# Optimization experiments

Hardware: AMD Instinct MI355X
Metric: run time of the kernel (lower is better)

Reference implementation:

```python
import jax, jax.numpy as jnp
import numpy as np

N_NODES = 100000
N_EDGES = 3200000
IN_CH = 128
HID = 8
HEADS = 8
NEG_SLOPE = 0.2  # PyG GATConv default


def setup_inputs() -> dict:
    key = jax.random.key(0)
    ks = jax.random.split(key, 12)
    s = 0.1
    return {
        "x": jax.random.normal(ks[0], (N_NODES, IN_CH), jnp.float32),
        "edge_index": jax.random.randint(ks[1], (2, N_EDGES), 0, N_NODES, dtype=jnp.int64),
        "W1": jax.random.normal(ks[2], (IN_CH, HEADS * HID), jnp.float32) * s,
        "a_src1": jax.random.normal(ks[3], (1, HEADS, HID), jnp.float32) * s,
        "a_dst1": jax.random.normal(ks[4], (1, HEADS, HID), jnp.float32) * s,
        "b1": jax.random.normal(ks[5], (HEADS * HID,), jnp.float32) * s,
        "W2": jax.random.normal(ks[6], (HEADS * HID, HID), jnp.float32) * s,
        "a_src2": jax.random.normal(ks[7], (1, 1, HID), jnp.float32) * s,
        "a_dst2": jax.random.normal(ks[8], (1, 1, HID), jnp.float32) * s,
        "b2": jax.random.normal(ks[9], (HID,), jnp.float32) * s,
        "Wc": jax.random.normal(ks[10], (HID, 2), jnp.float32) * s,
        "bc": jax.random.normal(ks[11], (2,), jnp.float32) * s,
    }


def gat_conv(x, src, dst, W, a_src, a_dst, b, concat):
    """PyG-style GATConv (eval mode, self-loops already appended to src/dst)."""
    n = x.shape[0]
    H, C = a_src.shape[1], a_src.shape[2]
    h = (x @ W).reshape(n, H, C)                       # [N,H,C]
    alpha_src = jnp.sum(h * a_src, axis=-1)            # [N,H]
    alpha_dst = jnp.sum(h * a_dst, axis=-1)            # [N,H]
    e = jax.nn.leaky_relu(alpha_src[src] + alpha_dst[dst], NEG_SLOPE)  # [E,H]
    # segment softmax over destination-node neighborhoods
    m = jax.ops.segment_max(e, dst, num_segments=n)    # [N,H]
    m = jnp.where(jnp.isfinite(m), m, 0.0)
    p = jnp.exp(e - m[dst])
    z = jax.ops.segment_sum(p, dst, num_segments=n)    # [N,H]
    alpha = p / (z[dst] + 1e-16)                       # [E,H]
    out = jax.ops.segment_sum(alpha[..., None] * h[src], dst, num_segments=n)  # [N,H,C]
    out = out.reshape(n, H * C) if concat else out.mean(axis=1)
    return out + b


def reference(x, edge_index, W1, a_src1, a_dst1, b1, W2, a_src2, a_dst2, b2, Wc, bc):
    n = x.shape[0]
    loops = jnp.arange(n, dtype=edge_index.dtype)
    src = jnp.concatenate([edge_index[0], loops])
    dst = jnp.concatenate([edge_index[1], loops])
    h = jax.nn.relu(gat_conv(x, src, dst, W1, a_src1, a_dst1, b1, concat=True))
    embeddings = gat_conv(h, src, dst, W2, a_src2, a_dst2, b2, concat=False)
    logits = embeddings @ Wc + bc
    return embeddings, logits
```

## Files before the change

### kernel.cpp

```cpp
#include <hip/hip_runtime.h>
#include <hip/hip_bf16.h>

#define NN 100000
#define IN_CH 128
#define HID 8
#define HEADS 8
#define HC 64
#define BSH 8
#define NBUCK ((NN + 255) >> 8)
#define NBLK 512
#define LOG2E 1.44269504088896340736f

__device__ __forceinline__ unsigned short f2bf(float f) {
    unsigned u = __float_as_uint(f);
    unsigned r = (u + 0x7fffu + ((u >> 16) & 1u)) >> 16;
    return (unsigned short)r;
}


__global__ __launch_bounds__(256) void k_bincount(const int* __restrict__ ei, int E, int ET,
                                                  int cpb, int* __restrict__ cnt) {
    __shared__ int h[NBUCK];
    for (int i = threadIdx.x; i < NBUCK; i += 256) h[i] = 0;
    __syncthreads();
    int beg = blockIdx.x * cpb, end = min(ET, beg + cpb);
    for (int t = beg + threadIdx.x; t < end; t += 256) {
        int d = (t < E) ? ei[E + t] : (t - E);
        atomicAdd(&h[d >> BSH], 1);
    }
    __syncthreads();
    for (int i = threadIdx.x; i < NBUCK; i += 256) cnt[i * NBLK + blockIdx.x] = h[i];
}

__global__ __launch_bounds__(256) void k_colscan(int* __restrict__ cnt, int* __restrict__ btot) {
    __shared__ int sd[256];
    int t = threadIdx.x;
    int* col = cnt + blockIdx.x * NBLK;
    int v0 = col[2 * t], v1 = col[2 * t + 1];
    int s = v0 + v1;
    sd[t] = s;
    __syncthreads();
    for (int off = 1; off < 256; off <<= 1) {
        int u = (t >= off) ? sd[t - off] : 0;
        __syncthreads();
        sd[t] += u;
        __syncthreads();
    }
    int excl = sd[t] - s;
    col[2 * t] = excl;
    col[2 * t + 1] = excl + v0;
    if (t == 255) btot[blockIdx.x] = excl + s;
}

__global__ __launch_bounds__(256) void k_bucketbase(const int* __restrict__ btot,
                                                    int* __restrict__ bbase,
                                                    int* __restrict__ row_ptr) {
    __shared__ int sd[256];
    int t = threadIdx.x;
    int v0 = (2 * t < NBUCK) ? btot[2 * t] : 0;
    int v1 = (2 * t + 1 < NBUCK) ? btot[2 * t + 1] : 0;
    int s = v0 + v1;
    sd[t] = s;
    __syncthreads();
    for (int off = 1; off < 256; off <<= 1) {
        int u = (t >= off) ? sd[t - off] : 0;
        __syncthreads();
        sd[t] += u;
        __syncthreads();
    }
    int excl = sd[t] - s;
    if (2 * t < NBUCK) bbase[2 * t] = excl;
    if (2 * t + 1 < NBUCK) bbase[2 * t + 1] = excl + v0;
    if (t == 255) { bbase[NBUCK] = excl + s; row_ptr[NN] = excl + s; }
}

__global__ __launch_bounds__(256) void k_binscatter(const int* __restrict__ ei, int E, int ET,
                                                    int cpb, const int* __restrict__ cnt,
                                                    const int* __restrict__ bbase,
                                                    int2* __restrict__ pairs) {
    __shared__ int cur[NBUCK];
    for (int i = threadIdx.x; i < NBUCK; i += 256)
        cur[i] = bbase[i] + cnt[i * NBLK + blockIdx.x];
    __syncthreads();
    int beg = blockIdx.x * cpb, end = min(ET, beg + cpb);
    for (int t = beg + threadIdx.x; t < end; t += 256) {
        int s, d;
        if (t < E) { s = ei[t]; d = ei[E + t]; } else { s = t - E; d = t - E; }
        int pos = atomicAdd(&cur[d >> BSH], 1);
        pairs[pos] = make_int2(s, d);
    }
}

__global__ __launch_bounds__(256) void k_bucketscatter(const int2* __restrict__ pairs,
                                                       const int* __restrict__ bbase,
                                                       int* __restrict__ row_ptr,
                                                       int* __restrict__ csr) {
    __shared__ int h[256];
    __shared__ int sd[256];
    int b = blockIdx.x;
    int t = threadIdx.x;
    int beg = bbase[b], end = bbase[b + 1];
    h[t] = 0;
    __syncthreads();
    for (int j = beg + t; j < end; j += 256) {
        int2 p = pairs[j];
        atomicAdd(&h[p.y & 255], 1);
    }
    __syncthreads();
    int v = h[t];
    sd[t] = v;
    __syncthreads();
    for (int off = 1; off < 256; off <<= 1) {
        int u = (t >= off) ? sd[t - off] : 0;
        __syncthreads();
        sd[t] += u;
        __syncthreads();
    }
    int excl = sd[t] - v;
    int node = (b << 8) + t;
    if (node < NN) row_ptr[node] = beg + excl;
    __syncthreads();
    h[t] = beg + excl;
    __syncthreads();
    for (int j = beg + t; j < end; j += 256) {
        int2 p = pairs[j];
        int pos = atomicAdd(&h[p.y & 255], 1);
        csr[pos] = p.x;
    }
}


__global__ __launch_bounds__(256) void k_gemm1(const float* __restrict__ x,
                                               const float* __restrict__ W1,
                                               const float* __restrict__ aS,
                                               const float* __restrict__ aD,
                                               unsigned short* __restrict__ h1bf,
                                               float* __restrict__ asrc1,
                                               float* __restrict__ adst1) {
    __shared__ float wl[IN_CH * HC];
    int tid = threadIdx.x;
    {
        const float4* Wg4 = (const float4*)W1;
        float4* wl4 = (float4*)wl;
#pragma unroll
        for (int i = 0; i < 8; ++i) wl4[tid + i * 256] = Wg4[tid + i * 256];
    }
    __syncthreads();
    int lane = tid & 63;
    int row = blockIdx.x * 16 + (tid >> 6) * 4 + (lane >> 4);
    int c0 = (lane & 15) * 4;
    const float4* xr = (const float4*)(x + (size_t)row * IN_CH);
    float4 acc = make_float4(0.f, 0.f, 0.f, 0.f);
#pragma unroll 4
    for (int kq = 0; kq < IN_CH / 4; ++kq) {
        float4 xv = xr[kq];
        const float4* wrow = (const float4*)(wl + (kq * 4) * HC + c0);
        float4 w0 = wrow[0];
        float4 w1 = wrow[HC / 4];
        float4 w2 = wrow[2 * (HC / 4)];
        float4 w3 = wrow[3 * (HC / 4)];
        acc.x += xv.x * w0.x + xv.y * w1.x + xv.z * w2.x + xv.w * w3.x;
        acc.y += xv.x * w0.y + xv.y * w1.y + xv.z * w2.y + xv.w * w3.y;
        acc.z += xv.x * w0.z + xv.y * w1.z + xv.z * w2.z + xv.w * w3.z;
        acc.w += xv.x * w0.w + xv.y * w1.w + xv.z * w2.w + xv.w * w3.w;
    }
    ushort4 hb;
    hb.x = f2bf(acc.x); hb.y = f2bf(acc.y); hb.z = f2bf(acc.z); hb.w = f2bf(acc.w);
    *(ushort4*)(h1bf + (size_t)row * HC + c0) = hb;
    int head = (lane & 15) >> 1;
    int cl = c0 & 7;
    const float* as = aS + head * 8 + cl;
    const float* ad = aD + head * 8 + cl;
    float ps = acc.x * as[0] + acc.y * as[1] + acc.z * as[2] + acc.w * as[3];
    float pd = acc.x * ad[0] + acc.y * ad[1] + acc.z * ad[2] + acc.w * ad[3];
    ps += __shfl_xor(ps, 1, 64);
    pd += __shfl_xor(pd, 1, 64);
    if ((lane & 1) == 0) {
        asrc1[row * 8 + head] = ps * LOG2E;
        adst1[row * 8 + head] = pd * LOG2E;
    }
}


__global__ __launch_bounds__(256) void k_agg1(const int* __restrict__ row_ptr,
                                              const int* __restrict__ csr,
                                              const float* __restrict__ asrc1,
                                              const float* __restrict__ adst1,
                                              const unsigned short* __restrict__ h1bf,
                                              const float* __restrict__ b1,
                                              const float* __restrict__ W2,
                                              const float* __restrict__ aS2,
                                              const float* __restrict__ aD2,
                                              float* __restrict__ h2,
                                              float* __restrict__ asrc2,
                                              float* __restrict__ adst2) {
    int tid = threadIdx.x;
    int lane = tid & 63;
    int slot = lane >> 3;
    int hl = lane & 7;
    float w2r[8];
#pragma unroll
    for (int i = 0; i < 8; ++i) w2r[i] = W2[(hl * 8 + i) * 8 + slot];
    float4 b0 = *(const float4*)(b1 + hl * 8);
    float4 b1v = *(const float4*)(b1 + hl * 8 + 4);
    float as2 = aS2[slot], ad2 = aD2[slot];
    const float4* h1v = (const float4*)h1bf;
    int nbase = (blockIdx.x * 4 + (tid >> 6)) * 4;
    for (int ni = 0; ni < 4; ++ni) {
        int n = nbase + ni;
        float adst = adst1[n * 8 + hl];
        int beg = row_ptr[n], end = row_ptr[n + 1];
        int nit = (end - beg + 7) >> 3;
        float z = 0.f;
        float4 accA = make_float4(0.f, 0.f, 0.f, 0.f);
        float4 accB = make_float4(0.f, 0.f, 0.f, 0.f);
        int j0 = beg + slot;
        bool v0 = j0 < end;
        int s0 = v0 ? csr[j0] : 0;
        int j1 = j0 + 8;
        bool v1 = j1 < end;
        int s1 = v1 ? csr[j1] : 0;
        float a0 = asrc1[(size_t)s0 * 8 + hl];
        float4 r0 = h1v[(size_t)s0 * 8 + hl];
        int jn = j1;
        for (int it = 0; it < nit; ++it) {
            int j2 = jn + 8;
            bool v2 = j2 < end;
            int s2 = v2 ? csr[j2] : 0;
            float a1 = asrc1[(size_t)s1 * 8 + hl];
            float4 r1 = h1v[(size_t)s1 * 8 + hl];
            float e = a0 + adst;
            e = fmaxf(e, 0.2f * e);
            float p = v0 ? exp2f(e) : 0.f;
            unsigned ux = __float_as_uint(r0.x), uy = __float_as_uint(r0.y);
            unsigned uz = __float_as_uint(r0.z), uw = __float_as_uint(r0.w);
            z += p;
            accA.x += p * __uint_as_float(ux << 16);
            accA.y += p * __uint_as_float(ux & 0xffff0000u);
            accA.z += p * __uint_as_float(uy << 16);
            accA.w += p * __uint_as_float(uy & 0xffff0000u);
            accB.x += p * __uint_as_float(uz << 16);
            accB.y += p * __uint_as_float(uz & 0xffff0000u);
            accB.z += p * __uint_as_float(uw << 16);
            accB.w += p * __uint_as_float(uw & 0xffff0000u);
            v0 = v1; a0 = a1; r0 = r1;
            v1 = v2; s1 = s2;
            jn = j2;
        }
#pragma unroll
        for (int off = 8; off <= 32; off <<= 1) {
            z += __shfl_xor(z, off, 64);
            accA.x += __shfl_xor(accA.x, off, 64);
            accA.y += __shfl_xor(accA.y, off, 64);
            accA.z += __shfl_xor(accA.z, off, 64);
            accA.w += __shfl_xor(accA.w, off, 64);
            accB.x += __shfl_xor(accB.x, off, 64);
            accB.y += __shfl_xor(accB.y, off, 64);
            accB.z += __shfl_xor(accB.z, off, 64);
            accB.w += __shfl_xor(accB.w, off, 64);
        }
        float inv = 1.f / (z + 1e-16f);
        float hr0 = fmaxf(accA.x * inv + b0.x, 0.f);
        float hr1 = fmaxf(accA.y * inv + b0.y, 0.f);
        float hr2 = fmaxf(accA.z * inv + b0.z, 0.f);
        float hr3 = fmaxf(accA.w * inv + b0.w, 0.f);
        float hr4 = fmaxf(accB.x * inv + b1v.x, 0.f);
        float hr5 = fmaxf(accB.y * inv + b1v.y, 0.f);
        float hr6 = fmaxf(accB.z * inv + b1v.z, 0.f);
        float hr7 = fmaxf(accB.w * inv + b1v.w, 0.f);
        float part = hr0 * w2r[0] + hr1 * w2r[1] + hr2 * w2r[2] + hr3 * w2r[3] +
                     hr4 * w2r[4] + hr5 * w2r[5] + hr6 * w2r[6] + hr7 * w2r[7];
        part += __shfl_xor(part, 1, 64);
        part += __shfl_xor(part, 2, 64);
        part += __shfl_xor(part, 4, 64);
        if (hl == 0) {
            h2[(size_t)n * 8 + slot] = part;
            float s2v = part * as2;
            float d2v = part * ad2;
            s2v += __shfl_xor(s2v, 8, 64);
            s2v += __shfl_xor(s2v, 16, 64);
            s2v += __shfl_xor(s2v, 32, 64);
            d2v += __shfl_xor(d2v, 8, 64);
            d2v += __shfl_xor(d2v, 16, 64);
            d2v += __shfl_xor(d2v, 32, 64);
            if (slot == 0) {
                asrc2[n] = s2v * LOG2E;
                adst2[n] = d2v * LOG2E;
            }
        }
    }
}


__global__ __launch_bounds__(256) void k_agg2(const int* __restrict__ row_ptr,
                                              const int* __restrict__ csr,
                                              const float* __restrict__ asrc2,
                                              const float* __restrict__ adst2,
                                              const float* __restrict__ h2,
                                              const float* __restrict__ b2,
                                              const float* __restrict__ Wc,
                                              const float* __restrict__ bc,
                                              float* __restrict__ out) {
    int tid = threadIdx.x;
    int lane = tid & 63;
    int n = blockIdx.x * 4 + (tid >> 6);
    int slot = lane >> 3;
    int sl = lane & 7;
    float adst = adst2[n];
    int beg = row_ptr[n], end = row_ptr[n + 1];
    int nit = (end - beg + 7) >> 3;
    float z = 0.f, acc = 0.f;
    int j0 = beg + slot;
    bool v0 = j0 < end;
    int s0 = v0 ? csr[j0] : 0;
    int j1 = j0 + 8;
    bool v1 = j1 < end;
    int s1 = v1 ? csr[j1] : 0;
    float a0 = asrc2[s0];
    float h0 = h2[(size_t)s0 * HID + sl];
    int jn = j1;
    for (int it = 0; it < nit; ++it) {
        int j2 = jn + 8;
        bool v2 = j2 < end;
        int s2 = v2 ? csr[j2] : 0;
        float a1 = asrc2[s1];
        float h1l = h2[(size_t)s1 * HID + sl];
        float e = a0 + adst;
        e = fmaxf(e, 0.2f * e);
        float p = v0 ? exp2f(e) : 0.f;
        z += p;
        acc += p * h0;
        v0 = v1; a0 = a1; h0 = h1l;
        v1 = v2; s1 = s2;
        jn = j2;
    }
#pragma unroll
    for (int off = 8; off <= 32; off <<= 1) {
        z += __shfl_xor(z, off, 64);
        acc += __shfl_xor(acc, off, 64);
    }
    float emb = acc / (z + 1e-16f) + b2[sl];
    if (slot == 0) out[(size_t)n * HID + sl] = emb;
    float t0 = emb * Wc[sl * 2 + 0];
    float t1 = emb * Wc[sl * 2 + 1];
    t0 += __shfl_xor(t0, 1, 64); t0 += __shfl_xor(t0, 2, 64); t0 += __shfl_xor(t0, 4, 64);
    t1 += __shfl_xor(t1, 1, 64); t1 += __shfl_xor(t1, 2, 64); t1 += __shfl_xor(t1, 4, 64);
    if (lane == 0) {
        out[(size_t)NN * HID + n * 2 + 0] = t0 + bc[0];
        out[(size_t)NN * HID + n * 2 + 1] = t1 + bc[1];
    }
}


extern "C" void kernel_launch(void* const* d_in, const int* in_sizes, int n_in,
                              void* d_out, int out_size, void* d_ws, size_t ws_size,
                              hipStream_t stream) {
    const float* x  = (const float*)d_in[0];
    const int*   ei = (const int*)d_in[1];
    const float* W1 = (const float*)d_in[2];
    const float* aS = (const float*)d_in[3];
    const float* aD = (const float*)d_in[4];
    const float* b1 = (const float*)d_in[5];
    const float* W2 = (const float*)d_in[6];
    const float* aS2 = (const float*)d_in[7];
    const float* aD2 = (const float*)d_in[8];
    const float* b2 = (const float*)d_in[9];
    const float* Wc = (const float*)d_in[10];
    const float* bc = (const float*)d_in[11];

    int E = in_sizes[1] / 2;
    int N = NN;
    int ET = E + N;
    int cpb = (ET + NBLK - 1) / NBLK;

    char* p = (char*)d_ws;
    auto alloc = [&](size_t bytes) -> char* {
        char* r = p;
        p += (bytes + 255) & ~(size_t)255;
        return r;
    };
    unsigned short* h1bf = (unsigned short*)alloc((size_t)N * HC * 2);
    float* asrc1  = (float*)alloc((size_t)N * 8 * 4);
    float* adst1  = (float*)alloc((size_t)N * 8 * 4);
    float* h2     = (float*)alloc((size_t)N * HID * 4);
    float* asrc2  = (float*)alloc((size_t)N * 4);
    float* adst2  = (float*)alloc((size_t)N * 4);
    int*   row_ptr= (int*)alloc((size_t)(N + 1) * 4);
    int*   cnt    = (int*)alloc((size_t)NBUCK * NBLK * 4);
    int*   btot   = (int*)alloc((size_t)NBUCK * 4);
    int*   bbase  = (int*)alloc((size_t)(NBUCK + 1) * 4);
    int*   csr    = (int*)alloc((size_t)ET * 4);
    int2*  pairs  = (int2*)alloc((size_t)ET * 8);

    k_bincount<<<NBLK, 256, 0, stream>>>(ei, E, ET, cpb, cnt);
    k_colscan<<<NBUCK, 256, 0, stream>>>(cnt, btot);
    k_bucketbase<<<1, 256, 0, stream>>>(btot, bbase, row_ptr);
    k_binscatter<<<NBLK, 256, 0, stream>>>(ei, E, ET, cpb, cnt, bbase, pairs);
    k_bucketscatter<<<NBUCK, 256, 0, stream>>>(pairs, bbase, row_ptr, csr);

    k_gemm1<<<N / 16, 256, 0, stream>>>(x, W1, aS, aD, h1bf, asrc1, adst1);
    k_agg1<<<N / 16, 256, 0, stream>>>(row_ptr, csr, asrc1, adst1, h1bf, b1,
                                       W2, aS2, aD2, h2, asrc2, adst2);
    k_agg2<<<N / 4, 256, 0, stream>>>(row_ptr, csr, asrc2, adst2, h2, b2, Wc, bc,
                                      (float*)d_out);
}
```

Baseline: 260.9 us.

## Quantize layer-1 features to int8, store h2 as bf16, pack sort pairs

Layer-1 projected features are stored as per-row int8 with an fp32 scale instead of bf16. This halves the gathered bytes per edge in the first aggregation. The layer-2 features are stored as bf16 instead of fp32, and the CSR sort pairs are packed into one 32-bit word (source shifted left 8, low byte of destination), with each bucket staged in shared memory when it fits. The int8 quantization adds accuracy error that may exceed the tolerance, and the packing assumes node indices fit in 24 bits.

Result: faster. 245.6 us (-5.9%).

```diff
diff --git a/kernel.cpp b/kernel.cpp
--- a/kernel.cpp
+++ b/kernel.cpp
@@ -9,6 +9,7 @@
 #define BSH 8
 #define NBUCK ((NN + 255) >> 8)
 #define NBLK 512
+#define PCAP 10240
 #define LOG2E 1.44269504088896340736f
 
 __device__ __forceinline__ unsigned short f2bf(float f) {
@@ -77,7 +78,7 @@
 __global__ __launch_bounds__(256) void k_binscatter(const int* __restrict__ ei, int E, int ET,
                                                     int cpb, const int* __restrict__ cnt,
                                                     const int* __restrict__ bbase,
-                                                    int2* __restrict__ pairs) {
+                                                    unsigned* __restrict__ pairs) {
     __shared__ int cur[NBUCK];
     for (int i = threadIdx.x; i < NBUCK; i += 256)
         cur[i] = bbase[i] + cnt[i * NBLK + blockIdx.x];
@@ -87,24 +88,29 @@
         int s, d;
         if (t < E) { s = ei[t]; d = ei[E + t]; } else { s = t - E; d = t - E; }
         int pos = atomicAdd(&cur[d >> BSH], 1);
-        pairs[pos] = make_int2(s, d);
-    }
-}
-
-__global__ __launch_bounds__(256) void k_bucketscatter(const int2* __restrict__ pairs,
+        pairs[pos] = ((unsigned)s << 8) | (unsigned)(d & 255);
+    }
+}
+
+__global__ __launch_bounds__(256) void k_bucketscatter(const unsigned* __restrict__ pairs,
                                                        const int* __restrict__ bbase,
                                                        int* __restrict__ row_ptr,
                                                        int* __restrict__ csr) {
+    __shared__ unsigned pl[PCAP];
     __shared__ int h[256];
     __shared__ int sd[256];
     int b = blockIdx.x;
     int t = threadIdx.x;
     int beg = bbase[b], end = bbase[b + 1];
+    int cntE = end - beg;
+    bool inl = cntE <= PCAP;
+    if (inl)
+        for (int j = t; j < cntE; j += 256) pl[j] = pairs[beg + j];
     h[t] = 0;
     __syncthreads();
-    for (int j = beg + t; j < end; j += 256) {
-        int2 p = pairs[j];
-        atomicAdd(&h[p.y & 255], 1);
+    for (int j = t; j < cntE; j += 256) {
+        unsigned pv = inl ? pl[j] : pairs[beg + j];
+        atomicAdd(&h[pv & 255u], 1);
     }
     __syncthreads();
     int v = h[t];
@@ -122,10 +128,10 @@
     __syncthreads();
     h[t] = beg + excl;
     __syncthreads();
-    for (int j = beg + t; j < end; j += 256) {
-        int2 p = pairs[j];
-        int pos = atomicAdd(&h[p.y & 255], 1);
-        csr[pos] = p.x;
+    for (int j = t; j < cntE; j += 256) {
+        unsigned pv = inl ? pl[j] : pairs[beg + j];
+        int pos = atomicAdd(&h[pv & 255u], 1);
+        csr[pos] = (int)(pv >> 8);
     }
 }
 
@@ -134,7 +140,8 @@
                                                const float* __restrict__ W1,
                                                const float* __restrict__ aS,
                                                const float* __restrict__ aD,
-                                               unsigned short* __restrict__ h1bf,
+                                               unsigned* __restrict__ h1q,
+                                               float* __restrict__ scale1,
                                                float* __restrict__ asrc1,
                                                float* __restrict__ adst1) {
     __shared__ float wl[IN_CH * HC];
@@ -164,9 +171,21 @@
         acc.z += xv.x * w0.z + xv.y * w1.z + xv.z * w2.z + xv.w * w3.z;
         acc.w += xv.x * w0.w + xv.y * w1.w + xv.z * w2.w + xv.w * w3.w;
     }
-    ushort4 hb;
-    hb.x = f2bf(acc.x); hb.y = f2bf(acc.y); hb.z = f2bf(acc.z); hb.w = f2bf(acc.w);
-    *(ushort4*)(h1bf + (size_t)row * HC + c0) = hb;
+    float am = fmaxf(fmaxf(fabsf(acc.x), fabsf(acc.y)), fmaxf(fabsf(acc.z), fabsf(acc.w)));
+    am = fmaxf(am, __shfl_xor(am, 1, 64));
+    am = fmaxf(am, __shfl_xor(am, 2, 64));
+    am = fmaxf(am, __shfl_xor(am, 4, 64));
+    am = fmaxf(am, __shfl_xor(am, 8, 64));
+    am = fmaxf(am, 1e-20f);
+    float qinv = 127.0f / am;
+    int q0 = __float2int_rn(acc.x * qinv);
+    int q1 = __float2int_rn(acc.y * qinv);
+    int q2 = __float2int_rn(acc.z * qinv);
+    int q3 = __float2int_rn(acc.w * qinv);
+    unsigned u = (unsigned)(q0 & 255) | ((unsigned)(q1 & 255) << 8) |
+                 ((unsigned)(q2 & 255) << 16) | ((unsigned)(q3 & 255) << 24);
+    h1q[row * 16 + (lane & 15)] = u;
+    if ((lane & 15) == 0) scale1[row] = am * (1.0f / 127.0f);
     int head = (lane & 15) >> 1;
     int cl = c0 & 7;
     const float* as = aS + head * 8 + cl;
@@ -186,12 +205,13 @@
                                               const int* __restrict__ csr,
                                               const float* __restrict__ asrc1,
                                               const float* __restrict__ adst1,
-                                              const unsigned short* __restrict__ h1bf,
+                                              const uint2* __restrict__ h1q,
+                                              const float* __restrict__ scale1,
                                               const float* __restrict__ b1,
                                               const float* __restrict__ W2,
                                               const float* __restrict__ aS2,
                                               const float* __restrict__ aD2,
-                                              float* __restrict__ h2,
+                                              unsigned short* __restrict__ h2bf,
                                               float* __restrict__ asrc2,
                                               float* __restrict__ adst2) {
     int tid = threadIdx.x;
@@ -204,7 +224,6 @@
     float4 b0 = *(const float4*)(b1 + hl * 8);
     float4 b1v = *(const float4*)(b1 + hl * 8 + 4);
     float as2 = aS2[slot], ad2 = aD2[slot];
-    const float4* h1v = (const float4*)h1bf;
     int nbase = (blockIdx.x * 4 + (tid >> 6)) * 4;
     for (int ni = 0; ni < 4; ++ni) {
         int n = nbase + ni;
@@ -221,29 +240,30 @@
         bool v1 = j1 < end;
         int s1 = v1 ? csr[j1] : 0;
         float a0 = asrc1[(size_t)s0 * 8 + hl];
-        float4 r0 = h1v[(size_t)s0 * 8 + hl];
+        float c0 = scale1[s0];
+        uint2 r0 = h1q[(size_t)s0 * 8 + hl];
         int jn = j1;
         for (int it = 0; it < nit; ++it) {
             int j2 = jn + 8;
             bool v2 = j2 < end;
             int s2 = v2 ? csr[j2] : 0;
             float a1 = asrc1[(size_t)s1 * 8 + hl];
-            float4 r1 = h1v[(size_t)s1 * 8 + hl];
+            float c1 = scale1[s1];
+            uint2 r1 = h1q[(size_t)s1 * 8 + hl];
             float e = a0 + adst;
             e = fmaxf(e, 0.2f * e);
             float p = v0 ? exp2f(e) : 0.f;
-            unsigned ux = __float_as_uint(r0.x), uy = __float_as_uint(r0.y);
-            unsigned uz = __float_as_uint(r0.z), uw = __float_as_uint(r0.w);
+            float ps = p * c0;
             z += p;
-            accA.x += p * __uint_as_float(ux << 16);
-            accA.y += p * __uint_as_float(ux & 0xffff0000u);
-            accA.z += p * __uint_as_float(uy << 16);
-            accA.w += p * __uint_as_float(uy & 0xffff0000u);
-            accB.x += p * __uint_as_float(uz << 16);
-            accB.y += p * __uint_as_float(uz & 0xffff0000u);
-            accB.z += p * __uint_as_float(uw << 16);
-            accB.w += p * __uint_as_float(uw & 0xffff0000u);
-            v0 = v1; a0 = a1; r0 = r1;
+            accA.x += ps * (float)(((int)(r0.x << 24)) >> 24);
+            accA.y += ps * (float)(((int)(r0.x << 16)) >> 24);
+            accA.z += ps * (float)(((int)(r0.x << 8)) >> 24);
+            accA.w += ps * (float)(((int)r0.x) >> 24);
+            accB.x += ps * (float)(((int)(r0.y << 24)) >> 24);
+            accB.y += ps * (float)(((int)(r0.y << 16)) >> 24);
+            accB.z += ps * (float)(((int)(r0.y << 8)) >> 24);
+            accB.w += ps * (float)(((int)r0.y) >> 24);
+            v0 = v1; a0 = a1; c0 = c1; r0 = r1;
             v1 = v2; s1 = s2;
             jn = j2;
         }
@@ -274,7 +294,7 @@
         part += __shfl_xor(part, 2, 64);
         part += __shfl_xor(part, 4, 64);
         if (hl == 0) {
-            h2[(size_t)n * 8 + slot] = part;
+            h2bf[(size_t)n * 8 + slot] = f2bf(part);
             float s2v = part * as2;
             float d2v = part * ad2;
             s2v += __shfl_xor(s2v, 8, 64);
@@ -296,7 +316,7 @@
                                               const int* __restrict__ csr,
                                               const float* __restrict__ asrc2,
                                               const float* __restrict__ adst2,
-                                              const float* __restrict__ h2,
+                                              const unsigned short* __restrict__ h2bf,
                                               const float* __restrict__ b2,
                                               const float* __restrict__ Wc,
                                               const float* __restrict__ bc,
@@ -317,20 +337,21 @@
     bool v1 = j1 < end;
     int s1 = v1 ? csr[j1] : 0;
     float a0 = asrc2[s0];
-    float h0 = h2[(size_t)s0 * HID + sl];
+    unsigned short u0 = h2bf[(size_t)s0 * 8 + sl];
     int jn = j1;
     for (int it = 0; it < nit; ++it) {
         int j2 = jn + 8;
         bool v2 = j2 < end;
         int s2 = v2 ? csr[j2] : 0;
         float a1 = asrc2[s1];
-        float h1l = h2[(size_t)s1 * HID + sl];
+        unsigned short u1 = h2bf[(size_t)s1 * 8 + sl];
         float e = a0 + adst;
         e = fmaxf(e, 0.2f * e);
         float p = v0 ? exp2f(e) : 0.f;
+        float h0 = __uint_as_float(((unsigned)u0) << 16);
         z += p;
         acc += p * h0;
-        v0 = v1; a0 = a1; h0 = h1l;
+        v0 = v1; a0 = a1; u0 = u1;
         v1 = v2; s1 = s2;
         jn = j2;
     }
@@ -379,18 +400,19 @@
         p += (bytes + 255) & ~(size_t)255;
         return r;
     };
-    unsigned short* h1bf = (unsigned short*)alloc((size_t)N * HC * 2);
-    float* asrc1  = (float*)alloc((size_t)N * 8 * 4);
-    float* adst1  = (float*)alloc((size_t)N * 8 * 4);
-    float* h2     = (float*)alloc((size_t)N * HID * 4);
-    float* asrc2  = (float*)alloc((size_t)N * 4);
-    float* adst2  = (float*)alloc((size_t)N * 4);
-    int*   row_ptr= (int*)alloc((size_t)(N + 1) * 4);
-    int*   cnt    = (int*)alloc((size_t)NBUCK * NBLK * 4);
-    int*   btot   = (int*)alloc((size_t)NBUCK * 4);
-    int*   bbase  = (int*)alloc((size_t)(NBUCK + 1) * 4);
-    int*   csr    = (int*)alloc((size_t)ET * 4);
-    int2*  pairs  = (int2*)alloc((size_t)ET * 8);
+    unsigned* h1q   = (unsigned*)alloc((size_t)N * 16 * 4);
+    float* scale1   = (float*)alloc((size_t)N * 4);
+    float* asrc1    = (float*)alloc((size_t)N * 8 * 4);
+    float* adst1    = (float*)alloc((size_t)N * 8 * 4);
+    unsigned short* h2bf = (unsigned short*)alloc((size_t)N * 8 * 2);
+    float* asrc2    = (float*)alloc((size_t)N * 4);
+    float* adst2    = (float*)alloc((size_t)N * 4);
+    int*   row_ptr  = (int*)alloc((size_t)(N + 1) * 4);
+    int*   cnt      = (int*)alloc((size_t)NBUCK * NBLK * 4);
+    int*   btot     = (int*)alloc((size_t)NBUCK * 4);
+    int*   bbase    = (int*)alloc((size_t)(NBUCK + 1) * 4);
+    int*   csr      = (int*)alloc((size_t)ET * 4);
+    unsigned* pairs = (unsigned*)alloc((size_t)ET * 4);
 
     k_bincount<<<NBLK, 256, 0, stream>>>(ei, E, ET, cpb, cnt);
     k_colscan<<<NBUCK, 256, 0, stream>>>(cnt, btot);
@@ -398,9 +420,9 @@
     k_binscatter<<<NBLK, 256, 0, stream>>>(ei, E, ET, cpb, cnt, bbase, pairs);
     k_bucketscatter<<<NBUCK, 256, 0, stream>>>(pairs, bbase, row_ptr, csr);
 
-    k_gemm1<<<N / 16, 256, 0, stream>>>(x, W1, aS, aD, h1bf, asrc1, adst1);
-    k_agg1<<<N / 16, 256, 0, stream>>>(row_ptr, csr, asrc1, adst1, h1bf, b1,
-                                       W2, aS2, aD2, h2, asrc2, adst2);
-    k_agg2<<<N / 4, 256, 0, stream>>>(row_ptr, csr, asrc2, adst2, h2, b2, Wc, bc,
+    k_gemm1<<<N / 16, 256, 0, stream>>>(x, W1, aS, aD, h1q, scale1, asrc1, adst1);
+    k_agg1<<<N / 16, 256, 0, stream>>>(row_ptr, csr, asrc1, adst1, (const uint2*)h1q,
+                                       scale1, b1, W2, aS2, aD2, h2bf, asrc2, adst2);
+    k_agg2<<<N / 4, 256, 0, stream>>>(row_ptr, csr, asrc2, adst2, h2bf, b2, Wc, bc,
                                       (float*)d_out);
 }
```
